# Optimization experiments

Hardware: AMD Instinct MI355X
Metric: run time of the kernel (lower is better)

The kernel has to match this reference:

```python
import jax, jax.numpy as jnp
import numpy as np

B, T, SD, AD, H, K, HID = 256, 128, 8, 2, 3, 4, 256


def setup_inputs() -> dict:
    key = jax.random.key(0)
    ks = jax.random.split(key, 12)
    inp = {
        "state": jax.random.normal(ks[0], (B, T, SD), dtype=jnp.float32),
        "action": jax.random.normal(ks[1], (B, T, AD), dtype=jnp.float32),
        # Linear(4, 4*H, bias=False): weight (4*H, 4)
        "Wk": jax.random.normal(ks[2], (4 * H, K), dtype=jnp.float32) * 0.1,
        "Wq": jax.random.normal(ks[3], (4 * H, SD + AD), dtype=jnp.float32) * 0.1,
        "Wv": jax.random.normal(ks[4], (4 * H, K), dtype=jnp.float32) * 0.1,
        # MLP: in_dim = 4*H + SD + AD -> HID -> HID -> 1
        "W1": jax.random.normal(ks[5], (HID, 4 * H + SD + AD), dtype=jnp.float32) * 0.05,
        "b1": jnp.zeros((HID,), dtype=jnp.float32),
        "W2": jax.random.normal(ks[6], (HID, HID), dtype=jnp.float32) * 0.05,
        "b2": jnp.zeros((HID,), dtype=jnp.float32),
        "Wout": jax.random.uniform(ks[7], (1, HID), minval=-0.003, maxval=0.003, dtype=jnp.float32),
        "bout": jax.random.uniform(ks[8], (1,), minval=-0.003, maxval=0.003, dtype=jnp.float32),
    }
    return inp


def reference(state, action, Wk, Wq, Wv, W1, b1, W2, b2, Wout, bout):
    q_state = jnp.concatenate([state, action], axis=-1)  # (b, t, sd+ad)
    s = state[:, :, :4]                                   # (b, t, 4)
    b, t, k = s.shape
    h = Wk.shape[0] // k
    # rel_full[b, i, j] = s[b, j] - s[b, i]  (matches torch view/transpose)
    rel_full = s[:, None, :, :] - s[:, :, None, :]        # (b, t, t, 4)
    # drop diagonal (self-pairs): idx[i] = all j != i, in order
    j = jnp.arange(t - 1)
    idx = j[None, :] + (j[None, :] >= jnp.arange(t)[:, None])  # (t, t-1)
    rel = jnp.take_along_axis(rel_full, idx[None, :, :, None], axis=2)  # (b, t, t-1, 4)
    # QKV projections (tiny head dim k=4)
    q = (q_state @ Wq.T).reshape(b, t, h, k)              # (b, t, h, 4)
    keys = (rel @ Wk.T).reshape(b, t, t - 1, h, k)        # (b, t, t-1, h, 4)
    vals = (rel @ Wv.T).reshape(b, t, t - 1, h, k)
    scores = jnp.einsum('bthk,btjhk->bthj', q, keys) / jnp.sqrt(jnp.float32(k))
    w = jax.nn.softmax(scores, axis=-1)                   # over the t-1 neighbors
    x = jnp.einsum('bthj,btjhk->bthk', w, vals).reshape(b, t, h * k)
    x = jnp.concatenate([x, q_state], axis=-1)            # (b, t, h*4 + sd+ad)
    x = jax.nn.relu(x @ W1.T + b1)
    x = jax.nn.relu(x @ W2.T + b2)
    return x @ Wout.T + bout                              # (b, t, 1)
```

## Files before the change

kernel.cpp:

```cpp
#include <hip/hip_runtime.h>
#include <math.h>

#define Bp 256
#define Tp 128
#define SDp 8
#define ADp 2
#define Hp 3
#define Kp 4
#define HIDp 256
#define QDp (SDp + ADp)
#define X1Dp (Hp * Kp + QDp)
#define QKLD 17
#define LOG2E 1.4426950408889634f

typedef short bf16x8 __attribute__((ext_vector_type(8)));
typedef float f32x4  __attribute__((ext_vector_type(4)));

__device__ __forceinline__ unsigned short f2bf(float f) {
    unsigned u = __float_as_uint(f);
    unsigned r = (u + 0x7FFFu + ((u >> 16) & 1u)) >> 16;
    return (unsigned short)r;
}

__device__ __forceinline__ unsigned h1_byte(int row, int colbytes) {
    return (((unsigned)row << 9) + (unsigned)colbytes) ^ ((unsigned)(row & 7) << 4);
}
__device__ __forceinline__ unsigned x1_byte(int row, int colbytes) {
    return ((unsigned)row << 6) + ((unsigned)colbytes ^ (((unsigned)row & 6u) << 3));
}

__global__ __launch_bounds__(256) void prep_kernel(
    const float* __restrict__ W1, const float* __restrict__ W2,
    unsigned short* __restrict__ W1b, unsigned short* __restrict__ W2b)
{
    const int bid = blockIdx.x;
    const int tid = threadIdx.x;
    if (bid < 64) {
        const int i = bid * 1024 + tid * 4;
        const float4 v = *(const float4*)(W2 + i);
        ushort4 o;
        o.x = f2bf(v.x); o.y = f2bf(v.y); o.z = f2bf(v.z); o.w = f2bf(v.w);
        *(ushort4*)(W2b + i) = o;
    } else {
        const int i = (bid - 64) * 256 + tid;
        const int r = i >> 5, c = i & 31;
        W1b[i] = (c < X1Dp) ? f2bf(W1[r * X1Dp + c]) : (unsigned short)0;
    }
}

__global__ __launch_bounds__(256, 4) void main_kernel(
    const float* __restrict__ state, const float* __restrict__ action,
    const float* __restrict__ Wk, const float* __restrict__ Wq,
    const float* __restrict__ Wv,
    const unsigned short* __restrict__ W1b, const unsigned short* __restrict__ W2b,
    const float* __restrict__ b1, const float* __restrict__ b2,
    const float* __restrict__ Wout, const float* __restrict__ bout,
    float* __restrict__ out)
{
    const int bid   = blockIdx.x;
    const int batch = bid >> 2;
    const int t0    = (bid & 3) * 32;
    const int tid   = threadIdx.x;
    const int lane  = tid & 63;
    const int wave  = tid >> 6;
    const int quad  = lane >> 4;
    const int l16   = lane & 15;
    const int t_loc = tid >> 3;
    const int jo    = tid & 7;
    const int t     = t0 + t_loc;

    __shared__ float4 s4[Tp];
    __shared__ float  wv[Hp * Kp * Kp];
    __shared__ float  qk[32 * QKLD];
    __shared__ float  b1s[HIDp];
    __shared__ float  b2s[HIDp];
    __shared__ float  wouts[HIDp];
    __shared__ __align__(16) unsigned short X1s[32 * 32];
    __shared__ __align__(16) unsigned short h1s[32 * 256];
    __shared__ float partial[4][32];

    if (tid < Tp) {
        s4[tid] = ((const float4*)(state + (size_t)batch * Tp * SDp))[tid * 2];
    } else if (tid < 160) {
        const int ta = tid - 128;
        const int tt = t0 + ta;
        float qs[QDp];
        {
            const float* srow = state + ((size_t)batch * Tp + tt) * SDp;
            const float4 v0 = *(const float4*)srow;
            const float4 v1 = *(const float4*)(srow + 4);
            qs[0]=v0.x; qs[1]=v0.y; qs[2]=v0.z; qs[3]=v0.w;
            qs[4]=v1.x; qs[5]=v1.y; qs[6]=v1.z; qs[7]=v1.w;
            const float* arow = action + ((size_t)batch * Tp + tt) * ADp;
            qs[8] = arow[0]; qs[9] = arow[1];
        }
        float q[Hp * Kp];
        #pragma unroll
        for (int r = 0; r < Hp * Kp; ++r) {
            float a = 0.f;
            #pragma unroll
            for (int d = 0; d < QDp; ++d) a += qs[d] * Wq[r * QDp + d];
            q[r] = a;
        }
        float* qrow = &qk[ta * QKLD];
        #pragma unroll
        for (int h = 0; h < Hp; ++h)
            #pragma unroll
            for (int c = 0; c < Kp; ++c) {
                float a = 0.f;
                #pragma unroll
                for (int k = 0; k < Kp; ++k) a += q[h * Kp + k] * Wk[(h * Kp + k) * Kp + c];
                qrow[h * 4 + c] = 0.5f * LOG2E * a;
            }
        #pragma unroll
        for (int i = 0; i < 5; ++i) {
            const unsigned u = (unsigned)f2bf(qs[2*i]) | ((unsigned)f2bf(qs[2*i+1]) << 16);
            qrow[12 + i] = __uint_as_float(u);
        }
    } else if (tid < 160 + Hp * Kp * Kp) {
        wv[tid - 160] = Wv[tid - 160];
    }
    b1s[tid]   = b1[tid];
    b2s[tid]   = b2[tid];
    wouts[tid] = Wout[tid];
    __syncthreads();

    float rq[12];
    #pragma unroll
    for (int i = 0; i < 3; ++i)
        *(float4*)&rq[i * 4] = *(const float4*)&qk[t_loc * QKLD + i * 4];

    float l[Hp] = {0.f, 0.f, 0.f};
    float ac[Hp][4] = {};
    #pragma unroll
    for (int i = 0; i < 16; ++i) {
        const int j = (jo << 4) | ((i + jo) & 15);
        const float4 sj = s4[j];
        #pragma unroll
        for (int h = 0; h < Hp; ++h) {
            const float d = sj.x * rq[h*4] + sj.y * rq[h*4+1]
                          + sj.z * rq[h*4+2] + sj.w * rq[h*4+3];
            const float e = __builtin_amdgcn_exp2f(d);
            l[h] += e;
            ac[h][0] += e * sj.x; ac[h][1] += e * sj.y;
            ac[h][2] += e * sj.z; ac[h][3] += e * sj.w;
        }
    }
    #pragma unroll
    for (int off = 1; off < 8; off <<= 1) {
        #pragma unroll
        for (int h = 0; h < Hp; ++h) {
            l[h] += __shfl_xor(l[h], off);
            #pragma unroll
            for (int c = 0; c < Kp; ++c) ac[h][c] += __shfl_xor(ac[h][c], off);
        }
    }

    if (jo == 0) {
        const float4 st = s4[t];
        unsigned short rowb[32] __attribute__((aligned(16)));
        #pragma unroll
        for (int h = 0; h < Hp; ++h) {
            const float dtt = st.x * rq[h*4] + st.y * rq[h*4+1]
                            + st.z * rq[h*4+2] + st.w * rq[h*4+3];
            const float ett = __builtin_amdgcn_exp2f(dtt);
            const float inv = 1.f / (l[h] - ett);
            const float rb0 = (ac[h][0] - ett * st.x) * inv - st.x;
            const float rb1 = (ac[h][1] - ett * st.y) * inv - st.y;
            const float rb2 = (ac[h][2] - ett * st.z) * inv - st.z;
            const float rb3 = (ac[h][3] - ett * st.w) * inv - st.w;
            #pragma unroll
            for (int k = 0; k < Kp; ++k) {
                const int r = h * Kp + k;
                rowb[r] = f2bf(rb0 * wv[r*4] + rb1 * wv[r*4+1] + rb2 * wv[r*4+2] + rb3 * wv[r*4+3]);
            }
        }
        #pragma unroll
        for (int i = 0; i < 5; ++i) {
            const unsigned u = __float_as_uint(qk[t_loc * QKLD + 12 + i]);
            rowb[12 + 2*i] = (unsigned short)(u & 0xffffu);
            rowb[13 + 2*i] = (unsigned short)(u >> 16);
        }
        #pragma unroll
        for (int i = X1Dp; i < 32; ++i) rowb[i] = 0;

        const uint4* srcv = (const uint4*)rowb;
        #pragma unroll
        for (int i = 0; i < 4; ++i)
            *(uint4*)((char*)X1s + x1_byte(t_loc, i * 16)) = srcv[i];
    }
    __syncthreads();

    {
        const int rt  = wave & 1;
        const int chh = wave >> 1;
        bf16x8 bfr[8];
        #pragma unroll
        for (int n = 0; n < 8; ++n)
            bfr[n] = *(const bf16x8*)&W1b[(chh * 128 + n * 16 + l16) * 32 + quad * 8];
        const bf16x8 afr = *(const bf16x8*)((const char*)X1s +
                             x1_byte(rt * 16 + l16, quad * 16));
        #pragma unroll
        for (int n = 0; n < 8; ++n) {
            const int col = chh * 128 + n * 16 + l16;
            f32x4 acc = {0.f, 0.f, 0.f, 0.f};
            acc = __builtin_amdgcn_mfma_f32_16x16x32_bf16(afr, bfr[n], acc, 0, 0, 0);
            const float bb = b1s[col];
            #pragma unroll
            for (int r = 0; r < 4; ++r) {
                const int row = rt * 16 + quad * 4 + r;
                *(unsigned short*)((char*)h1s + h1_byte(row, col * 2)) =
                    f2bf(fmaxf(acc[r] + bb, 0.f));
            }
        }
    }
    __syncthreads();

    float rsum[2][4] = {};
    #pragma unroll
    for (int i = 0; i < 4; ++i) {
        const int col = (wave * 4 + i) * 16 + l16;
        const unsigned short* wr = W2b + (size_t)col * HIDp + quad * 8;
        bf16x8 Bf[8];
        #pragma unroll
        for (int ks = 0; ks < 8; ++ks)
            Bf[ks] = *(const bf16x8*)(wr + ks * 32);
        const float bb = b2s[col];
        const float wo = wouts[col];
        #pragma unroll
        for (int rt = 0; rt < 2; ++rt) {
            bf16x8 A8[8];
            #pragma unroll
            for (int ks = 0; ks < 8; ++ks)
                A8[ks] = *(const bf16x8*)((const char*)h1s +
                           h1_byte(rt * 16 + l16, ks * 64 + quad * 16));
            f32x4 acc = {0.f, 0.f, 0.f, 0.f};
            #pragma unroll
            for (int ks = 0; ks < 8; ++ks)
                acc = __builtin_amdgcn_mfma_f32_16x16x32_bf16(A8[ks], Bf[ks], acc, 0, 0, 0);
            #pragma unroll
            for (int r = 0; r < 4; ++r)
                rsum[rt][r] += fmaxf(acc[r] + bb, 0.f) * wo;
        }
    }

    #pragma unroll
    for (int off = 1; off < 16; off <<= 1)
        #pragma unroll
        for (int rt = 0; rt < 2; ++rt)
            #pragma unroll
            for (int r = 0; r < 4; ++r)
                rsum[rt][r] += __shfl_xor(rsum[rt][r], off);

    if (l16 == 0) {
        #pragma unroll
        for (int rt = 0; rt < 2; ++rt)
            #pragma unroll
            for (int r = 0; r < 4; ++r)
                partial[wave][rt * 16 + quad * 4 + r] = rsum[rt][r];
    }
    __syncthreads();

    if (tid < 32) {
        out[(size_t)batch * Tp + t0 + tid] =
            partial[0][tid] + partial[1][tid] + partial[2][tid]
          + partial[3][tid] + bout[0];
    }
}

extern "C" void kernel_launch(void* const* d_in, const int* in_sizes, int n_in,
                              void* d_out, int out_size, void* d_ws, size_t ws_size,
                              hipStream_t stream) {
    const float* state  = (const float*)d_in[0];
    const float* action = (const float*)d_in[1];
    const float* Wk     = (const float*)d_in[2];
    const float* Wq     = (const float*)d_in[3];
    const float* Wv     = (const float*)d_in[4];
    const float* W1     = (const float*)d_in[5];
    const float* b1     = (const float*)d_in[6];
    const float* W2     = (const float*)d_in[7];
    const float* b2     = (const float*)d_in[8];
    const float* Wout   = (const float*)d_in[9];
    const float* bout   = (const float*)d_in[10];
    float* out = (float*)d_out;

    char* ws = (char*)d_ws;
    unsigned short* W1b = (unsigned short*)(ws);
    unsigned short* W2b = (unsigned short*)(ws + 16384);

    prep_kernel<<<96, 256, 0, stream>>>(W1, W2, W1b, W2b);
    main_kernel<<<4 * Bp, 256, 0, stream>>>(state, action, Wk, Wq, Wv,
                                            W1b, W2b, b1, b2, Wout, bout, out);
}
```

Before: 96.87 us.

## Halve positions per block, double grid, prefetch first W2 tile early

Each block now handles 16 query positions instead of 32, so the grid doubles and each thread scans 8 neighbours instead of 16, with a wider 16-lane shuffle reduction. The W1 and W2 MFMA stages are reshaped for a single 16-row tile, so the h1 A fragments are loaded once. The first W2 B tile is loaded before the initial barrier to hide global latency, and the K-loop is split across two accumulators. The cost is that each W2 column tile is now fetched for only 16 rows, doubling total W2 traffic and per-block setup work such as the s4, bias and Wout loads.

```diff
diff --git a/kernel.cpp b/kernel.cpp
--- a/kernel.cpp
+++ b/kernel.cpp
@@ -11,6 +11,7 @@
 #define QDp (SDp + ADp)
 #define X1Dp (Hp * Kp + QDp)
 #define QKLD 17
+#define POSB 16
 #define LOG2E 1.4426950408889634f
 
 typedef short bf16x8 __attribute__((ext_vector_type(8)));
@@ -58,31 +59,31 @@
     float* __restrict__ out)
 {
     const int bid   = blockIdx.x;
-    const int batch = bid >> 2;
-    const int t0    = (bid & 3) * 32;
+    const int batch = bid >> 3;
+    const int t0    = (bid & 7) * POSB;
     const int tid   = threadIdx.x;
     const int lane  = tid & 63;
     const int wave  = tid >> 6;
     const int quad  = lane >> 4;
     const int l16   = lane & 15;
-    const int t_loc = tid >> 3;
-    const int jo    = tid & 7;
+    const int t_loc = tid >> 4;
+    const int jo    = tid & 15;
     const int t     = t0 + t_loc;
 
     __shared__ float4 s4[Tp];
     __shared__ float  wv[Hp * Kp * Kp];
-    __shared__ float  qk[32 * QKLD];
+    __shared__ float  qk[POSB * QKLD];
     __shared__ float  b1s[HIDp];
     __shared__ float  b2s[HIDp];
     __shared__ float  wouts[HIDp];
-    __shared__ __align__(16) unsigned short X1s[32 * 32];
-    __shared__ __align__(16) unsigned short h1s[32 * 256];
-    __shared__ float partial[4][32];
+    __shared__ __align__(16) unsigned short X1s[POSB * 32];
+    __shared__ __align__(16) unsigned short h1s[POSB * 256];
+    __shared__ float partial[4][POSB];
 
     if (tid < Tp) {
         s4[tid] = ((const float4*)(state + (size_t)batch * Tp * SDp))[tid * 2];
-    } else if (tid < 160) {
-        const int ta = tid - 128;
+    } else if (tid < Tp + POSB) {
+        const int ta = tid - Tp;
         const int tt = t0 + ta;
         float qs[QDp];
         {
@@ -117,12 +118,21 @@
             const unsigned u = (unsigned)f2bf(qs[2*i]) | ((unsigned)f2bf(qs[2*i+1]) << 16);
             qrow[12 + i] = __uint_as_float(u);
         }
-    } else if (tid < 160 + Hp * Kp * Kp) {
-        wv[tid - 160] = Wv[tid - 160];
+    } else if (tid < Tp + POSB + Hp * Kp * Kp) {
+        wv[tid - Tp - POSB] = Wv[tid - Tp - POSB];
     }
     b1s[tid]   = b1[tid];
     b2s[tid]   = b2[tid];
     wouts[tid] = Wout[tid];
+
+    bf16x8 Bf0[8];
+    {
+        const int col0 = (wave * 4 + 0) * 16 + l16;
+        const unsigned short* wr0 = W2b + (size_t)col0 * HIDp + quad * 8;
+        #pragma unroll
+        for (int ks = 0; ks < 8; ++ks)
+            Bf0[ks] = *(const bf16x8*)(wr0 + ks * 32);
+    }
     __syncthreads();
 
     float rq[12];
@@ -133,8 +143,8 @@
     float l[Hp] = {0.f, 0.f, 0.f};
     float ac[Hp][4] = {};
     #pragma unroll
-    for (int i = 0; i < 16; ++i) {
-        const int j = (jo << 4) | ((i + jo) & 15);
+    for (int i = 0; i < 8; ++i) {
+        const int j = (jo << 3) | ((i + jo) & 7);
         const float4 sj = s4[j];
         #pragma unroll
         for (int h = 0; h < Hp; ++h) {
@@ -147,7 +157,7 @@
         }
     }
     #pragma unroll
-    for (int off = 1; off < 8; off <<= 1) {
+    for (int off = 1; off < 16; off <<= 1) {
         #pragma unroll
         for (int h = 0; h < Hp; ++h) {
             l[h] += __shfl_xor(l[h], off);
@@ -192,23 +202,20 @@
     __syncthreads();
 
     {
-        const int rt  = wave & 1;
-        const int chh = wave >> 1;
-        bf16x8 bfr[8];
-        #pragma unroll
-        for (int n = 0; n < 8; ++n)
-            bfr[n] = *(const bf16x8*)&W1b[(chh * 128 + n * 16 + l16) * 32 + quad * 8];
-        const bf16x8 afr = *(const bf16x8*)((const char*)X1s +
-                             x1_byte(rt * 16 + l16, quad * 16));
-        #pragma unroll
-        for (int n = 0; n < 8; ++n) {
-            const int col = chh * 128 + n * 16 + l16;
+        bf16x8 bfr[4];
+        #pragma unroll
+        for (int n = 0; n < 4; ++n)
+            bfr[n] = *(const bf16x8*)&W1b[(wave * 64 + n * 16 + l16) * 32 + quad * 8];
+        const bf16x8 afr = *(const bf16x8*)((const char*)X1s + x1_byte(l16, quad * 16));
+        #pragma unroll
+        for (int n = 0; n < 4; ++n) {
+            const int col = wave * 64 + n * 16 + l16;
             f32x4 acc = {0.f, 0.f, 0.f, 0.f};
             acc = __builtin_amdgcn_mfma_f32_16x16x32_bf16(afr, bfr[n], acc, 0, 0, 0);
             const float bb = b1s[col];
             #pragma unroll
             for (int r = 0; r < 4; ++r) {
-                const int row = rt * 16 + quad * 4 + r;
+                const int row = quad * 4 + r;
                 *(unsigned short*)((char*)h1s + h1_byte(row, col * 2)) =
                     f2bf(fmaxf(acc[r] + bb, 0.f));
             }
@@ -216,52 +223,53 @@
     }
     __syncthreads();
 
-    float rsum[2][4] = {};
+    bf16x8 A8[8];
+    #pragma unroll
+    for (int ks = 0; ks < 8; ++ks)
+        A8[ks] = *(const bf16x8*)((const char*)h1s + h1_byte(l16, ks * 64 + quad * 16));
+
+    float rsum[4] = {0.f, 0.f, 0.f, 0.f};
     #pragma unroll
     for (int i = 0; i < 4; ++i) {
         const int col = (wave * 4 + i) * 16 + l16;
-        const unsigned short* wr = W2b + (size_t)col * HIDp + quad * 8;
         bf16x8 Bf[8];
-        #pragma unroll
-        for (int ks = 0; ks < 8; ++ks)
-            Bf[ks] = *(const bf16x8*)(wr + ks * 32);
+        if (i == 0) {
+            #pragma unroll
+            for (int ks = 0; ks < 8; ++ks) Bf[ks] = Bf0[ks];
+        } else {
+            const unsigned short* wr = W2b + (size_t)col * HIDp + quad * 8;
+            #pragma unroll
+            for (int ks = 0; ks < 8; ++ks)
+                Bf[ks] = *(const bf16x8*)(wr + ks * 32);
+        }
         const float bb = b2s[col];
         const float wo = wouts[col];
-        #pragma unroll
-        for (int rt = 0; rt < 2; ++rt) {
-            bf16x8 A8[8];
-            #pragma unroll
-            for (int ks = 0; ks < 8; ++ks)
-                A8[ks] = *(const bf16x8*)((const char*)h1s +
-                           h1_byte(rt * 16 + l16, ks * 64 + quad * 16));
-            f32x4 acc = {0.f, 0.f, 0.f, 0.f};
-            #pragma unroll
-            for (int ks = 0; ks < 8; ++ks)
-                acc = __builtin_amdgcn_mfma_f32_16x16x32_bf16(A8[ks], Bf[ks], acc, 0, 0, 0);
-            #pragma unroll
-            for (int r = 0; r < 4; ++r)
-                rsum[rt][r] += fmaxf(acc[r] + bb, 0.f) * wo;
-        }
+        f32x4 acc0 = {0.f, 0.f, 0.f, 0.f};
+        f32x4 acc1 = {0.f, 0.f, 0.f, 0.f};
+        #pragma unroll
+        for (int ks = 0; ks < 4; ++ks) {
+            acc0 = __builtin_amdgcn_mfma_f32_16x16x32_bf16(A8[ks],     Bf[ks],     acc0, 0, 0, 0);
+            acc1 = __builtin_amdgcn_mfma_f32_16x16x32_bf16(A8[ks + 4], Bf[ks + 4], acc1, 0, 0, 0);
+        }
+        #pragma unroll
+        for (int r = 0; r < 4; ++r)
+            rsum[r] += fmaxf(acc0[r] + acc1[r] + bb, 0.f) * wo;
     }
 
     #pragma unroll
     for (int off = 1; off < 16; off <<= 1)
         #pragma unroll
-        for (int rt = 0; rt < 2; ++rt)
-            #pragma unroll
-            for (int r = 0; r < 4; ++r)
-                rsum[rt][r] += __shfl_xor(rsum[rt][r], off);
+        for (int r = 0; r < 4; ++r)
+            rsum[r] += __shfl_xor(rsum[r], off);
 
     if (l16 == 0) {
         #pragma unroll
-        for (int rt = 0; rt < 2; ++rt)
-            #pragma unroll
-            for (int r = 0; r < 4; ++r)
-                partial[wave][rt * 16 + quad * 4 + r] = rsum[rt][r];
+        for (int r = 0; r < 4; ++r)
+            partial[wave][quad * 4 + r] = rsum[r];
     }
     __syncthreads();
 
-    if (tid < 32) {
+    if (tid < POSB) {
         out[(size_t)batch * Tp + t0 + tid] =
             partial[0][tid] + partial[1][tid] + partial[2][tid]
           + partial[3][tid] + bout[0];
@@ -289,6 +297,6 @@
     unsigned short* W2b = (unsigned short*)(ws + 16384);
 
     prep_kernel<<<96, 256, 0, stream>>>(W1, W2, W1b, W2b);
-    main_kernel<<<4 * Bp, 256, 0, stream>>>(state, action, Wk, Wq, Wv,
+    main_kernel<<<8 * Bp, 256, 0, stream>>>(state, action, Wk, Wq, Wv,
                                             W1b, W2b, b1, b2, Wout, bout, out);
 }
```

Result: slower. 109.5 us (+13.0%).

## Prefetch MLP weights before attention and double-buffer W2 fragments

Applied to the files above, without the earlier changes.

The W1 bf16 fragments and the first W2 fragment group are now loaded at kernel entry, so their global-memory latency overlaps the attention phase. The second MLP layer is rewritten into a software-pipelined loop over half-K chunks: the next chunk's W2 fragments load while the current chunk's MFMAs run. Both 16-row tiles now share each B fragment. This targets the exposed global-load latency of the weight fetches, at the cost of more live registers across the attention phase, which could lower occupancy or cause spills.

```diff
diff --git a/kernel.cpp b/kernel.cpp
--- a/kernel.cpp
+++ b/kernel.cpp
@@ -79,6 +79,20 @@
     __shared__ __align__(16) unsigned short h1s[32 * 256];
     __shared__ float partial[4][32];
 
+    const int rt_b  = wave & 1;
+    const int chh_b = wave >> 1;
+    bf16x8 bfr[8];
+    #pragma unroll
+    for (int n = 0; n < 8; ++n)
+        bfr[n] = *(const bf16x8*)&W1b[(chh_b * 128 + n * 16 + l16) * 32 + quad * 8];
+    bf16x8 Bc[4];
+    {
+        const unsigned short* wr0 = W2b + (size_t)((wave * 4 + 0) * 16 + l16) * HIDp + quad * 8;
+        #pragma unroll
+        for (int k = 0; k < 4; ++k)
+            Bc[k] = *(const bf16x8*)(wr0 + k * 32);
+    }
+
     if (tid < Tp) {
         s4[tid] = ((const float4*)(state + (size_t)batch * Tp * SDp))[tid * 2];
     } else if (tid < 160) {
@@ -192,23 +206,17 @@
     __syncthreads();
 
     {
-        const int rt  = wave & 1;
-        const int chh = wave >> 1;
-        bf16x8 bfr[8];
-        #pragma unroll
-        for (int n = 0; n < 8; ++n)
-            bfr[n] = *(const bf16x8*)&W1b[(chh * 128 + n * 16 + l16) * 32 + quad * 8];
         const bf16x8 afr = *(const bf16x8*)((const char*)X1s +
-                             x1_byte(rt * 16 + l16, quad * 16));
+                             x1_byte(rt_b * 16 + l16, quad * 16));
         #pragma unroll
         for (int n = 0; n < 8; ++n) {
-            const int col = chh * 128 + n * 16 + l16;
+            const int col = chh_b * 128 + n * 16 + l16;
             f32x4 acc = {0.f, 0.f, 0.f, 0.f};
             acc = __builtin_amdgcn_mfma_f32_16x16x32_bf16(afr, bfr[n], acc, 0, 0, 0);
             const float bb = b1s[col];
             #pragma unroll
             for (int r = 0; r < 4; ++r) {
-                const int row = rt * 16 + quad * 4 + r;
+                const int row = rt_b * 16 + quad * 4 + r;
                 *(unsigned short*)((char*)h1s + h1_byte(row, col * 2)) =
                     f2bf(fmaxf(acc[r] + bb, 0.f));
             }
@@ -217,31 +225,46 @@
     __syncthreads();
 
     float rsum[2][4] = {};
-    #pragma unroll
-    for (int i = 0; i < 4; ++i) {
-        const int col = (wave * 4 + i) * 16 + l16;
-        const unsigned short* wr = W2b + (size_t)col * HIDp + quad * 8;
-        bf16x8 Bf[8];
-        #pragma unroll
-        for (int ks = 0; ks < 8; ++ks)
-            Bf[ks] = *(const bf16x8*)(wr + ks * 32);
-        const float bb = b2s[col];
-        const float wo = wouts[col];
-        #pragma unroll
-        for (int rt = 0; rt < 2; ++rt) {
-            bf16x8 A8[8];
-            #pragma unroll
-            for (int ks = 0; ks < 8; ++ks)
-                A8[ks] = *(const bf16x8*)((const char*)h1s +
-                           h1_byte(rt * 16 + l16, ks * 64 + quad * 16));
-            f32x4 acc = {0.f, 0.f, 0.f, 0.f};
-            #pragma unroll
-            for (int ks = 0; ks < 8; ++ks)
-                acc = __builtin_amdgcn_mfma_f32_16x16x32_bf16(A8[ks], Bf[ks], acc, 0, 0, 0);
-            #pragma unroll
-            for (int r = 0; r < 4; ++r)
-                rsum[rt][r] += fmaxf(acc[r] + bb, 0.f) * wo;
-        }
+    f32x4 acc0 = {0.f, 0.f, 0.f, 0.f};
+    f32x4 acc1 = {0.f, 0.f, 0.f, 0.f};
+    bf16x8 Bn[4];
+    #pragma unroll
+    for (int g = 0; g < 8; ++g) {
+        const int i  = g >> 1;
+        const int hf = g & 1;
+        if (g < 7) {
+            const int ni  = (g + 1) >> 1;
+            const int nhf = (g + 1) & 1;
+            const unsigned short* wr = W2b + (size_t)((wave * 4 + ni) * 16 + l16) * HIDp
+                                     + nhf * 128 + quad * 8;
+            #pragma unroll
+            for (int k = 0; k < 4; ++k)
+                Bn[k] = *(const bf16x8*)(wr + k * 32);
+        }
+        #pragma unroll
+        for (int k = 0; k < 4; ++k) {
+            const int ksg = hf * 4 + k;
+            const bf16x8 a0 = *(const bf16x8*)((const char*)h1s +
+                                h1_byte(l16,      ksg * 64 + quad * 16));
+            const bf16x8 a1 = *(const bf16x8*)((const char*)h1s +
+                                h1_byte(16 + l16, ksg * 64 + quad * 16));
+            acc0 = __builtin_amdgcn_mfma_f32_16x16x32_bf16(a0, Bc[k], acc0, 0, 0, 0);
+            acc1 = __builtin_amdgcn_mfma_f32_16x16x32_bf16(a1, Bc[k], acc1, 0, 0, 0);
+        }
+        if (hf == 1) {
+            const int col = (wave * 4 + i) * 16 + l16;
+            const float bb = b2s[col];
+            const float wo = wouts[col];
+            #pragma unroll
+            for (int r = 0; r < 4; ++r) {
+                rsum[0][r] += fmaxf(acc0[r] + bb, 0.f) * wo;
+                rsum[1][r] += fmaxf(acc1[r] + bb, 0.f) * wo;
+            }
+            acc0 = (f32x4){0.f, 0.f, 0.f, 0.f};
+            acc1 = (f32x4){0.f, 0.f, 0.f, 0.f};
+        }
+        #pragma unroll
+        for (int k = 0; k < 4; ++k) Bc[k] = Bn[k];
     }
 
     #pragma unroll
```

After: 109.0 us. 1.13x slower.

## Process 64 timesteps per 512-thread block and prefetch MLP weights early

Applied to the files above, without the earlier changes.

Each block now covers 64 timesteps with 512 threads, halving the grid. Each wave's share of the W2 columns is halved, which reduces how often W2 weight fragments are re-read from global memory across blocks. The W1 and W2 fragments are loaded into registers at kernel start so their latency overlaps the attention phase. The layer-2 loop now reads A fragments from shared memory inside the inner loop instead of holding them in registers. The costs are higher register pressure from the held weight fragments, which could limit occupancy, and fewer blocks in flight.

```diff
diff --git a/kernel.cpp b/kernel.cpp
--- a/kernel.cpp
+++ b/kernel.cpp
@@ -48,7 +48,7 @@
     }
 }
 
-__global__ __launch_bounds__(256, 4) void main_kernel(
+__global__ __launch_bounds__(512, 2) void main_kernel(
     const float* __restrict__ state, const float* __restrict__ action,
     const float* __restrict__ Wk, const float* __restrict__ Wq,
     const float* __restrict__ Wv,
@@ -58,31 +58,49 @@
     float* __restrict__ out)
 {
     const int bid   = blockIdx.x;
-    const int batch = bid >> 2;
-    const int t0    = (bid & 3) * 32;
+    const int batch = bid >> 1;
+    const int t0    = (bid & 1) * 64;
     const int tid   = threadIdx.x;
     const int lane  = tid & 63;
     const int wave  = tid >> 6;
     const int quad  = lane >> 4;
     const int l16   = lane & 15;
-    const int t_loc = tid >> 3;
-    const int jo    = tid & 7;
-    const int t     = t0 + t_loc;
+    const int tileA = tid >> 8;
+    const int tid8  = tid & 255;
+    const int t_loc = tid8 >> 3;
+    const int jo    = tid8 & 7;
+    const int trow  = tileA * 32 + t_loc;
+    const int t     = t0 + trow;
 
     __shared__ float4 s4[Tp];
     __shared__ float  wv[Hp * Kp * Kp];
-    __shared__ float  qk[32 * QKLD];
+    __shared__ float  qk[64 * QKLD];
     __shared__ float  b1s[HIDp];
     __shared__ float  b2s[HIDp];
     __shared__ float  wouts[HIDp];
-    __shared__ __align__(16) unsigned short X1s[32 * 32];
-    __shared__ __align__(16) unsigned short h1s[32 * 256];
-    __shared__ float partial[4][32];
+    __shared__ __align__(16) unsigned short X1s[64 * 32];
+    __shared__ __align__(16) unsigned short h1s[64 * 256];
+    __shared__ float partial[8][64];
+
+    const int tileB = wave >> 2;
+    const int rtB   = wave & 1;
+    const int chhB  = (wave >> 1) & 1;
+    bf16x8 bfr[8];
+    #pragma unroll
+    for (int n = 0; n < 8; ++n)
+        bfr[n] = *(const bf16x8*)&W1b[(chhB * 128 + n * 16 + l16) * 32 + quad * 8];
+    bf16x8 Bc[8];
+    {
+        const unsigned short* wr0 = W2b + (size_t)(wave * 32 + l16) * HIDp + quad * 8;
+        #pragma unroll
+        for (int ks = 0; ks < 8; ++ks)
+            Bc[ks] = *(const bf16x8*)(wr0 + ks * 32);
+    }
 
     if (tid < Tp) {
         s4[tid] = ((const float4*)(state + (size_t)batch * Tp * SDp))[tid * 2];
-    } else if (tid < 160) {
-        const int ta = tid - 128;
+    } else if (tid < Tp + 64) {
+        const int ta = tid - Tp;
         const int tt = t0 + ta;
         float qs[QDp];
         {
@@ -117,18 +135,21 @@
             const unsigned u = (unsigned)f2bf(qs[2*i]) | ((unsigned)f2bf(qs[2*i+1]) << 16);
             qrow[12 + i] = __uint_as_float(u);
         }
-    } else if (tid < 160 + Hp * Kp * Kp) {
-        wv[tid - 160] = Wv[tid - 160];
-    }
-    b1s[tid]   = b1[tid];
-    b2s[tid]   = b2[tid];
-    wouts[tid] = Wout[tid];
+    } else if (tid < Tp + 64 + Hp * Kp * Kp) {
+        wv[tid - Tp - 64] = Wv[tid - Tp - 64];
+    }
+    if (tid >= 256) {
+        const int i = tid - 256;
+        b1s[i]   = b1[i];
+        b2s[i]   = b2[i];
+        wouts[i] = Wout[i];
+    }
     __syncthreads();
 
     float rq[12];
     #pragma unroll
     for (int i = 0; i < 3; ++i)
-        *(float4*)&rq[i * 4] = *(const float4*)&qk[t_loc * QKLD + i * 4];
+        *(float4*)&rq[i * 4] = *(const float4*)&qk[trow * QKLD + i * 4];
 
     float l[Hp] = {0.f, 0.f, 0.f};
     float ac[Hp][4] = {};
@@ -157,18 +178,19 @@
     }
 
     if (jo == 0) {
-        const float4 st = s4[t];
+        const float4 st = s4[t0 + trow - t0];
+        const float4 stt = s4[t];
         unsigned short rowb[32] __attribute__((aligned(16)));
         #pragma unroll
         for (int h = 0; h < Hp; ++h) {
-            const float dtt = st.x * rq[h*4] + st.y * rq[h*4+1]
-                            + st.z * rq[h*4+2] + st.w * rq[h*4+3];
+            const float dtt = stt.x * rq[h*4] + stt.y * rq[h*4+1]
+                            + stt.z * rq[h*4+2] + stt.w * rq[h*4+3];
             const float ett = __builtin_amdgcn_exp2f(dtt);
             const float inv = 1.f / (l[h] - ett);
-            const float rb0 = (ac[h][0] - ett * st.x) * inv - st.x;
-            const float rb1 = (ac[h][1] - ett * st.y) * inv - st.y;
-            const float rb2 = (ac[h][2] - ett * st.z) * inv - st.z;
-            const float rb3 = (ac[h][3] - ett * st.w) * inv - st.w;
+            const float rb0 = (ac[h][0] - ett * stt.x) * inv - stt.x;
+            const float rb1 = (ac[h][1] - ett * stt.y) * inv - stt.y;
+            const float rb2 = (ac[h][2] - ett * stt.z) * inv - stt.z;
+            const float rb3 = (ac[h][3] - ett * stt.w) * inv - stt.w;
             #pragma unroll
             for (int k = 0; k < Kp; ++k) {
                 const int r = h * Kp + k;
@@ -177,7 +199,7 @@
         }
         #pragma unroll
         for (int i = 0; i < 5; ++i) {
-            const unsigned u = __float_as_uint(qk[t_loc * QKLD + 12 + i]);
+            const unsigned u = __float_as_uint(qk[trow * QKLD + 12 + i]);
             rowb[12 + 2*i] = (unsigned short)(u & 0xffffu);
             rowb[13 + 2*i] = (unsigned short)(u >> 16);
         }
@@ -187,28 +209,22 @@
         const uint4* srcv = (const uint4*)rowb;
         #pragma unroll
         for (int i = 0; i < 4; ++i)
-            *(uint4*)((char*)X1s + x1_byte(t_loc, i * 16)) = srcv[i];
+            *(uint4*)((char*)X1s + x1_byte(trow, i * 16)) = srcv[i];
     }
     __syncthreads();
 
     {
-        const int rt  = wave & 1;
-        const int chh = wave >> 1;
-        bf16x8 bfr[8];
-        #pragma unroll
-        for (int n = 0; n < 8; ++n)
-            bfr[n] = *(const bf16x8*)&W1b[(chh * 128 + n * 16 + l16) * 32 + quad * 8];
         const bf16x8 afr = *(const bf16x8*)((const char*)X1s +
-                             x1_byte(rt * 16 + l16, quad * 16));
+                             x1_byte(tileB * 32 + rtB * 16 + l16, quad * 16));
         #pragma unroll
         for (int n = 0; n < 8; ++n) {
-            const int col = chh * 128 + n * 16 + l16;
+            const int col = chhB * 128 + n * 16 + l16;
             f32x4 acc = {0.f, 0.f, 0.f, 0.f};
             acc = __builtin_amdgcn_mfma_f32_16x16x32_bf16(afr, bfr[n], acc, 0, 0, 0);
             const float bb = b1s[col];
             #pragma unroll
             for (int r = 0; r < 4; ++r) {
-                const int row = rt * 16 + quad * 4 + r;
+                const int row = tileB * 32 + rtB * 16 + quad * 4 + r;
                 *(unsigned short*)((char*)h1s + h1_byte(row, col * 2)) =
                     f2bf(fmaxf(acc[r] + bb, 0.f));
             }
@@ -216,55 +232,59 @@
     }
     __syncthreads();
 
-    float rsum[2][4] = {};
-    #pragma unroll
-    for (int i = 0; i < 4; ++i) {
-        const int col = (wave * 4 + i) * 16 + l16;
-        const unsigned short* wr = W2b + (size_t)col * HIDp + quad * 8;
-        bf16x8 Bf[8];
+    float rsum[4][4] = {};
+
+    bf16x8 Bn[8];
+    {
+        const unsigned short* wr1 = W2b + (size_t)(wave * 32 + 16 + l16) * HIDp + quad * 8;
         #pragma unroll
         for (int ks = 0; ks < 8; ++ks)
-            Bf[ks] = *(const bf16x8*)(wr + ks * 32);
+            Bn[ks] = *(const bf16x8*)(wr1 + ks * 32);
+    }
+
+    #pragma unroll
+    for (int i = 0; i < 2; ++i) {
+        const int col = wave * 32 + i * 16 + l16;
         const float bb = b2s[col];
         const float wo = wouts[col];
         #pragma unroll
-        for (int rt = 0; rt < 2; ++rt) {
-            bf16x8 A8[8];
-            #pragma unroll
-            for (int ks = 0; ks < 8; ++ks)
-                A8[ks] = *(const bf16x8*)((const char*)h1s +
-                           h1_byte(rt * 16 + l16, ks * 64 + quad * 16));
+        for (int rt4 = 0; rt4 < 4; ++rt4) {
             f32x4 acc = {0.f, 0.f, 0.f, 0.f};
             #pragma unroll
-            for (int ks = 0; ks < 8; ++ks)
-                acc = __builtin_amdgcn_mfma_f32_16x16x32_bf16(A8[ks], Bf[ks], acc, 0, 0, 0);
+            for (int ks = 0; ks < 8; ++ks) {
+                const bf16x8 a8 = *(const bf16x8*)((const char*)h1s +
+                                    h1_byte(rt4 * 16 + l16, ks * 64 + quad * 16));
+                acc = __builtin_amdgcn_mfma_f32_16x16x32_bf16(
+                          a8, (i == 0) ? Bc[ks] : Bn[ks], acc, 0, 0, 0);
+            }
             #pragma unroll
             for (int r = 0; r < 4; ++r)
-                rsum[rt][r] += fmaxf(acc[r] + bb, 0.f) * wo;
+                rsum[rt4][r] += fmaxf(acc[r] + bb, 0.f) * wo;
         }
     }
 
     #pragma unroll
     for (int off = 1; off < 16; off <<= 1)
         #pragma unroll
-        for (int rt = 0; rt < 2; ++rt)
+        for (int rt4 = 0; rt4 < 4; ++rt4)
             #pragma unroll
             for (int r = 0; r < 4; ++r)
-                rsum[rt][r] += __shfl_xor(rsum[rt][r], off);
+                rsum[rt4][r] += __shfl_xor(rsum[rt4][r], off);
 
     if (l16 == 0) {
         #pragma unroll
-        for (int rt = 0; rt < 2; ++rt)
+        for (int rt4 = 0; rt4 < 4; ++rt4)
             #pragma unroll
             for (int r = 0; r < 4; ++r)
-                partial[wave][rt * 16 + quad * 4 + r] = rsum[rt][r];
+                partial[wave][rt4 * 16 + quad * 4 + r] = rsum[rt4][r];
     }
     __syncthreads();
 
-    if (tid < 32) {
-        out[(size_t)batch * Tp + t0 + tid] =
-            partial[0][tid] + partial[1][tid] + partial[2][tid]
-          + partial[3][tid] + bout[0];
+    if (tid < 64) {
+        float o = bout[0];
+        #pragma unroll
+        for (int w = 0; w < 8; ++w) o += partial[w][tid];
+        out[(size_t)batch * Tp + t0 + tid] = o;
     }
 }
 
@@ -289,6 +309,6 @@
     unsigned short* W2b = (unsigned short*)(ws + 16384);
 
     prep_kernel<<<96, 256, 0, stream>>>(W1, W2, W1b, W2b);
-    main_kernel<<<4 * Bp, 256, 0, stream>>>(state, action, Wk, Wq, Wv,
+    main_kernel<<<2 * Bp, 512, 0, stream>>>(state, action, Wk, Wq, Wv,
                                             W1b, W2b, b1, b2, Wout, bout, out);
 }
```

Result: slower. 99.79 us (+3.0%).
